# Kernel tuning notes

Measured on AMD Instinct MI355X. Metric: run time of the kernel, lower is better.

The kernel has to match this reference:

```python
import jax, jax.numpy as jnp
import numpy as np

N_NODES = 50000
N_EDGES = 1600000
D_IN = 512
D_OUT = 512


def setup_inputs() -> dict:
    key = jax.random.key(0)
    k1, k2, k3, k4, k5, k6 = jax.random.split(key, 6)
    stdv = 1.0 / np.sqrt(D_OUT)
    x = jax.random.normal(k1, (N_NODES, D_IN), dtype=jnp.float32)
    weight = jax.random.uniform(k2, (D_IN, D_OUT), dtype=jnp.float32, minval=-stdv, maxval=stdv)
    bias = jax.random.uniform(k3, (1, D_OUT), dtype=jnp.float32, minval=-stdv, maxval=stdv)
    edge_val = jax.random.uniform(k4, (N_EDGES,), dtype=jnp.float32)
    edge_row = jax.random.randint(k5, (N_EDGES,), 0, N_NODES, dtype=jnp.int64)
    edge_col = jax.random.randint(k6, (N_EDGES,), 0, N_NODES, dtype=jnp.int64)
    return {"x": x, "weight": weight, "bias": bias,
            "edge_val": edge_val, "edge_row": edge_row, "edge_col": edge_col}


def reference(x, weight, bias, edge_val, edge_row, edge_col):
    # hidden = X @ W  : [N, D_OUT] dense GEMM
    hidden = jnp.matmul(x, weight)
    # spmm: out[i] = sum over edges (i <- j) of adj_val * hidden[j]
    msgs = edge_val[:, None] * hidden[edge_col]            # [E, D_OUT]
    out = jax.ops.segment_sum(msgs, edge_row, num_segments=N_NODES)
    return out + bias
```

## Files before the change

kernel.cpp:

```cpp
#include <hip/hip_runtime.h>

typedef short short8 __attribute__((ext_vector_type(8)));
typedef float v4f   __attribute__((ext_vector_type(4)));

#define N_NODES 50000
#define N_EDGES 1600000
#define DIM     512
#define SCAN_NB 49

__device__ __forceinline__ float bf2f(unsigned short u) {
    unsigned int x = ((unsigned int)u) << 16;
    return __uint_as_float(x);
}
__device__ __forceinline__ unsigned short f2bf(float f) {
    unsigned int x = __float_as_uint(f);
    unsigned int r = x + 0x7fffu + ((x >> 16) & 1u);
    return (unsigned short)(r >> 16);
}

__global__ void detect_kernel(const unsigned int* __restrict__ xw,
                              const int* __restrict__ erow,
                              int* __restrict__ flags) {
    __shared__ int cbf, cz;
    if (threadIdx.x == 0) { cbf = 0; cz = 0; }
    __syncthreads();
    int lb = 0, lz = 0;
    for (int i = threadIdx.x; i < 1024; i += 256) {
        unsigned int w = xw[i];
        unsigned int e0 = (w >> 7) & 0xFFu;
        unsigned int e1 = (w >> 23) & 0xFFu;
        if (e0 >= 0x70u && e0 <= 0x8Fu && e1 >= 0x70u && e1 <= 0x8Fu) lb++;
        if (erow[2 * i + 1] == 0) lz++;
    }
    atomicAdd(&cbf, lb);
    atomicAdd(&cz, lz);
    __syncthreads();
    if (threadIdx.x == 0) {
        flags[0] = (cbf > 512) ? 1 : 0;
        flags[1] = (cz > 512) ? 1 : 0;
    }
}

__global__ void transpose_w(const void* __restrict__ Wv,
                            unsigned short* __restrict__ Wt,
                            const int* __restrict__ flags) {
    __shared__ unsigned short tile[32][33];
    const bool fb = flags[0] != 0;
    int bx = blockIdx.x * 32, by = blockIdx.y * 32;
    int tx = threadIdx.x, ty = threadIdx.y;
    if (fb) {
        const unsigned short* W = (const unsigned short*)Wv;
        for (int r = ty; r < 32; r += 8)
            tile[r][tx] = W[(by + r) * DIM + bx + tx];
    } else {
        const float* W = (const float*)Wv;
        for (int r = ty; r < 32; r += 8)
            tile[r][tx] = f2bf(W[(by + r) * DIM + bx + tx]);
    }
    __syncthreads();
    for (int r = ty; r < 32; r += 8)
        Wt[(bx + r) * DIM + by + tx] = tile[tx][r];
}

#define TM 128
#define TN 128
#define BK 32
#define LP 40

__global__ __launch_bounds__(256) void gemm_kernel(
        const void* __restrict__ Xv,
        const unsigned short* __restrict__ Wt,
        unsigned short* __restrict__ H,
        const int* __restrict__ flags) {
    __shared__ unsigned short lA[TM * LP];
    __shared__ unsigned short lB[TN * LP];

    const bool fb = flags[0] != 0;
    const unsigned short* Xb = (const unsigned short*)Xv;
    const float*          Xf = (const float*)Xv;

    const int t = threadIdx.x;
    const int mBase = blockIdx.y * TM;
    const int nBase = blockIdx.x * TN;
    const int w = t >> 6, lane = t & 63;
    const int lr = lane & 15, quad = lane >> 4;
    const int wr = w >> 1, wc = w & 1;

    v4f acc[4][4];
    #pragma unroll
    for (int i = 0; i < 4; ++i)
        #pragma unroll
        for (int j = 0; j < 4; ++j) acc[i][j] = (v4f)0.0f;

    for (int k0 = 0; k0 < DIM; k0 += BK) {
        #pragma unroll
        for (int rep = 0; rep < 2; ++rep) {
            int idx = rep * 256 + t;
            int r = idx >> 2;
            int cc = (idx & 3) * 8;
            int grow = mBase + r; if (grow >= N_NODES) grow = N_NODES - 1;
            size_t goff = (size_t)grow * DIM + k0 + cc;
            if (fb) {
                uint4 av = *(const uint4*)(Xb + goff);
                *(uint4*)(&lA[r * LP + cc]) = av;
            } else {
                float4 a0 = *(const float4*)(Xf + goff);
                float4 a1 = *(const float4*)(Xf + goff + 4);
                uint4 av;
                av.x = (unsigned int)f2bf(a0.x) | ((unsigned int)f2bf(a0.y) << 16);
                av.y = (unsigned int)f2bf(a0.z) | ((unsigned int)f2bf(a0.w) << 16);
                av.z = (unsigned int)f2bf(a1.x) | ((unsigned int)f2bf(a1.y) << 16);
                av.w = (unsigned int)f2bf(a1.z) | ((unsigned int)f2bf(a1.w) << 16);
                *(uint4*)(&lA[r * LP + cc]) = av;
            }
            uint4 bv = *(const uint4*)(Wt + (size_t)(nBase + r) * DIM + k0 + cc);
            *(uint4*)(&lB[r * LP + cc]) = bv;
        }
        __syncthreads();

        short8 bfr[4];
        #pragma unroll
        for (int j = 0; j < 4; ++j)
            bfr[j] = *(const short8*)(&lB[(wc * 64 + j * 16 + lr) * LP + quad * 8]);
        #pragma unroll
        for (int i = 0; i < 4; ++i) {
            short8 a = *(const short8*)(&lA[(wr * 64 + i * 16 + lr) * LP + quad * 8]);
            #pragma unroll
            for (int j = 0; j < 4; ++j)
                acc[i][j] = __builtin_amdgcn_mfma_f32_16x16x32_bf16(a, bfr[j], acc[i][j], 0, 0, 0);
        }
        __syncthreads();
    }

    #pragma unroll
    for (int i = 0; i < 4; ++i) {
        #pragma unroll
        for (int j = 0; j < 4; ++j) {
            #pragma unroll
            for (int r = 0; r < 4; ++r) {
                int gm = mBase + wr * 64 + i * 16 + quad * 4 + r;
                int gn = nBase + wc * 64 + j * 16 + lr;
                if (gm < N_NODES)
                    H[(size_t)gm * DIM + gn] = f2bf(acc[i][j][r]);
            }
        }
    }
}

__global__ void hist_kernel(const int* __restrict__ row, int* __restrict__ cnt,
                            const int* __restrict__ flags) {
    const bool f64 = flags[1] != 0;
    int i = blockIdx.x * 256 + threadIdx.x;
    if (i < N_EDGES) {
        int r = f64 ? row[2 * (size_t)i] : row[i];
        atomicAdd(&cnt[r], 1);
    }
}

__global__ __launch_bounds__(256) void scan1_kernel(const int* __restrict__ cnt,
                                                    int* __restrict__ bsum) {
    __shared__ int sh[256];
    const int b = blockIdx.x, t = threadIdx.x;
    int base = b * 1024 + t * 4;
    int s = 0;
    #pragma unroll
    for (int k = 0; k < 4; ++k) {
        int i = base + k;
        if (i < N_NODES) s += cnt[i];
    }
    sh[t] = s;
    __syncthreads();
    for (int off = 128; off > 0; off >>= 1) {
        if (t < off) sh[t] += sh[t + off];
        __syncthreads();
    }
    if (t == 0) bsum[b] = sh[0];
}

__global__ void scan2_kernel(const int* __restrict__ bsum, int* __restrict__ boff,
                             int* __restrict__ start) {
    if (threadIdx.x == 0) {
        int run = 0;
        for (int b = 0; b < SCAN_NB; ++b) { boff[b] = run; run += bsum[b]; }
        start[N_NODES] = N_EDGES;
    }
}

__global__ __launch_bounds__(256) void scan3_kernel(const int* __restrict__ cnt,
                                                    const int* __restrict__ boff,
                                                    int* __restrict__ start,
                                                    int* __restrict__ cursor) {
    __shared__ int sh[256];
    const int b = blockIdx.x, t = threadIdx.x;
    int base = b * 1024 + t * 4;
    int v[4];
    #pragma unroll
    for (int k = 0; k < 4; ++k) {
        int i = base + k;
        v[k] = (i < N_NODES) ? cnt[i] : 0;
    }
    int tsum = v[0] + v[1] + v[2] + v[3];
    sh[t] = tsum;
    __syncthreads();
    for (int off = 1; off < 256; off <<= 1) {
        int x = (t >= off) ? sh[t - off] : 0;
        __syncthreads();
        sh[t] += x;
        __syncthreads();
    }
    int excl = sh[t] - tsum + boff[b];
    #pragma unroll
    for (int k = 0; k < 4; ++k) {
        int i = base + k;
        if (i < N_NODES) { start[i] = excl; cursor[i] = excl; }
        excl += v[k];
    }
}

__global__ void scatter_kernel(const int* __restrict__ row, const int* __restrict__ col,
                               const void* __restrict__ valv,
                               int* __restrict__ cursor,
                               int2* __restrict__ sCV,
                               const int* __restrict__ flags) {
    const bool fb  = flags[0] != 0;
    const bool f64 = flags[1] != 0;
    int i = blockIdx.x * 256 + threadIdx.x;
    if (i < N_EDGES) {
        int r = f64 ? row[2 * (size_t)i] : row[i];
        int c = f64 ? col[2 * (size_t)i] : col[i];
        float v = fb ? bf2f(((const unsigned short*)valv)[i])
                     : ((const float*)valv)[i];
        int p = atomicAdd(&cursor[r], 1);
        int2 cv; cv.x = c; cv.y = __float_as_int(v);
        sCV[p] = cv;
    }
}

__global__ __launch_bounds__(256) void gather_kernel(
        const int* __restrict__ start, const int2* __restrict__ sCV,
        const unsigned short* __restrict__ H,
        const void* __restrict__ biasv, void* __restrict__ outv,
        const int* __restrict__ flags) {
    const bool fb = flags[0] != 0;
    const int node = blockIdx.x;
    const int t = threadIdx.x;
    const int s = start[node], e = start[node + 1];
    float a0 = 0.f, a1 = 0.f;
    #pragma unroll 4
    for (int p = s; p < e; ++p) {
        int2 cv = sCV[p];
        float v = __int_as_float(cv.y);
        unsigned int h = *(const unsigned int*)(H + (size_t)cv.x * DIM + t * 2);
        a0 = fmaf(v, bf2f((unsigned short)(h & 0xffffu)), a0);
        a1 = fmaf(v, bf2f((unsigned short)(h >> 16)), a1);
    }
    if (fb) {
        unsigned int bb = ((const unsigned int*)biasv)[t];
        a0 += bf2f((unsigned short)(bb & 0xffffu));
        a1 += bf2f((unsigned short)(bb >> 16));
        unsigned int o = (unsigned int)f2bf(a0) | ((unsigned int)f2bf(a1) << 16);
        ((unsigned int*)outv)[(size_t)node * (DIM / 2) + t] = o;
    } else {
        const float* bf = (const float*)biasv;
        a0 += bf[t * 2];
        a1 += bf[t * 2 + 1];
        float2 o; o.x = a0; o.y = a1;
        *(float2*)((float*)outv + (size_t)node * DIM + t * 2) = o;
    }
}

extern "C" void kernel_launch(void* const* d_in, const int* in_sizes, int n_in,
                              void* d_out, int out_size, void* d_ws, size_t ws_size,
                              hipStream_t stream) {
    const void* X    = d_in[0];
    const void* W    = d_in[1];
    const void* bias = d_in[2];
    const void* eval = d_in[3];
    const int*  erow = (const int*)d_in[4];
    const int*  ecol = (const int*)d_in[5];

    char* w = (char*)d_ws;
    size_t o = 0;
    int* flags = (int*)(w + o); o += 256;
    unsigned short* hidden = (unsigned short*)(w + o); o += (size_t)N_NODES * DIM * 2;
    int2*  sCV    = (int2*)(w + o);  o += (size_t)N_EDGES * 8;
    int*   cnt    = (int*)(w + o);   o += 200704;
    int*   start  = (int*)(w + o);   o += 200704;
    int*   cursor = (int*)(w + o);   o += 200704;
    unsigned short* Wt = (unsigned short*)(w + o); o += (size_t)DIM * DIM * 2;
    int*   bsum   = (int*)(w + o);   o += 256;
    int*   boff   = (int*)(w + o);   o += 256;

    hipMemsetAsync(cnt, 0, N_NODES * sizeof(int), stream);

    detect_kernel<<<1, 256, 0, stream>>>((const unsigned int*)X, erow, flags);
    transpose_w<<<dim3(16, 16), dim3(32, 8), 0, stream>>>(W, Wt, flags);
    gemm_kernel<<<dim3(DIM / TN, (N_NODES + TM - 1) / TM), 256, 0, stream>>>(X, Wt, hidden, flags);
    hist_kernel<<<(N_EDGES + 255) / 256, 256, 0, stream>>>(erow, cnt, flags);
    scan1_kernel<<<SCAN_NB, 256, 0, stream>>>(cnt, bsum);
    scan2_kernel<<<1, 64, 0, stream>>>(bsum, boff, start);
    scan3_kernel<<<SCAN_NB, 256, 0, stream>>>(cnt, boff, start, cursor);
    scatter_kernel<<<(N_EDGES + 255) / 256, 256, 0, stream>>>(erow, ecol, eval, cursor, sCV, flags);
    gather_kernel<<<N_NODES, 256, 0, stream>>>(start, sCV, hidden, bias, d_out, flags);
}
```

Baseline: 700.9 us.

## Pre-convert X to bf16, merge scan kernels, widen gather to 4 columns per thread

Adds a convert_x pass that writes X as bf16 into workspace once, so the GEMM reads bf16 instead of converting fp32 in each of its four column-block passes over X. The single-threaded scan2 kernel is folded into scan3, where each block sums the preceding block totals itself. The gather kernel now uses 128 threads per node, each loading and accumulating 4 bf16 values with vector loads and stores. Costs are an extra full read and write of X and a dependency on sufficient workspace size, which falls back to the old path if it is not available.

```diff
diff --git a/kernel.cpp b/kernel.cpp
--- a/kernel.cpp
+++ b/kernel.cpp
@@ -12,10 +12,10 @@
     unsigned int x = ((unsigned int)u) << 16;
     return __uint_as_float(x);
 }
-__device__ __forceinline__ unsigned short f2bf(float f) {
+__device__ __forceinline__ unsigned int f2bfu(float f) {
     unsigned int x = __float_as_uint(f);
     unsigned int r = x + 0x7fffu + ((x >> 16) & 1u);
-    return (unsigned short)(r >> 16);
+    return r >> 16;
 }
 
 __global__ void detect_kernel(const unsigned int* __restrict__ xw,
@@ -39,6 +39,22 @@
         flags[0] = (cbf > 512) ? 1 : 0;
         flags[1] = (cz > 512) ? 1 : 0;
     }
+}
+
+__global__ __launch_bounds__(256) void convert_x(const void* __restrict__ Xv,
+                                                 unsigned short* __restrict__ Xc,
+                                                 const int* __restrict__ flags) {
+    if (flags[0] != 0) return;
+    const float* Xf = (const float*)Xv;
+    size_t i = ((size_t)blockIdx.x * 256 + threadIdx.x) * 8;
+    float4 f0 = *(const float4*)(Xf + i);
+    float4 f1 = *(const float4*)(Xf + i + 4);
+    uint4 o;
+    o.x = f2bfu(f0.x) | (f2bfu(f0.y) << 16);
+    o.y = f2bfu(f0.z) | (f2bfu(f0.w) << 16);
+    o.z = f2bfu(f1.x) | (f2bfu(f1.y) << 16);
+    o.w = f2bfu(f1.z) | (f2bfu(f1.w) << 16);
+    *(uint4*)(Xc + i) = o;
 }
 
 __global__ void transpose_w(const void* __restrict__ Wv,
@@ -55,7 +71,7 @@
     } else {
         const float* W = (const float*)Wv;
         for (int r = ty; r < 32; r += 8)
-            tile[r][tx] = f2bf(W[(by + r) * DIM + bx + tx]);
+            tile[r][tx] = (unsigned short)f2bfu(W[(by + r) * DIM + bx + tx]);
     }
     __syncthreads();
     for (int r = ty; r < 32; r += 8)
@@ -69,6 +85,8 @@
 
 __global__ __launch_bounds__(256) void gemm_kernel(
         const void* __restrict__ Xv,
+        const unsigned short* __restrict__ Xc,
+        const int have_xc,
         const unsigned short* __restrict__ Wt,
         unsigned short* __restrict__ H,
         const int* __restrict__ flags) {
@@ -76,7 +94,8 @@
     __shared__ unsigned short lB[TN * LP];
 
     const bool fb = flags[0] != 0;
-    const unsigned short* Xb = (const unsigned short*)Xv;
+    const bool bfp = fb || (have_xc != 0);
+    const unsigned short* Xb = fb ? (const unsigned short*)Xv : Xc;
     const float*          Xf = (const float*)Xv;
 
     const int t = threadIdx.x;
@@ -100,17 +119,17 @@
             int cc = (idx & 3) * 8;
             int grow = mBase + r; if (grow >= N_NODES) grow = N_NODES - 1;
             size_t goff = (size_t)grow * DIM + k0 + cc;
-            if (fb) {
+            if (bfp) {
                 uint4 av = *(const uint4*)(Xb + goff);
                 *(uint4*)(&lA[r * LP + cc]) = av;
             } else {
                 float4 a0 = *(const float4*)(Xf + goff);
                 float4 a1 = *(const float4*)(Xf + goff + 4);
                 uint4 av;
-                av.x = (unsigned int)f2bf(a0.x) | ((unsigned int)f2bf(a0.y) << 16);
-                av.y = (unsigned int)f2bf(a0.z) | ((unsigned int)f2bf(a0.w) << 16);
-                av.z = (unsigned int)f2bf(a1.x) | ((unsigned int)f2bf(a1.y) << 16);
-                av.w = (unsigned int)f2bf(a1.z) | ((unsigned int)f2bf(a1.w) << 16);
+                av.x = f2bfu(a0.x) | (f2bfu(a0.y) << 16);
+                av.y = f2bfu(a0.z) | (f2bfu(a0.w) << 16);
+                av.z = f2bfu(a1.x) | (f2bfu(a1.y) << 16);
+                av.w = f2bfu(a1.z) | (f2bfu(a1.w) << 16);
                 *(uint4*)(&lA[r * LP + cc]) = av;
             }
             uint4 bv = *(const uint4*)(Wt + (size_t)(nBase + r) * DIM + k0 + cc);
@@ -141,7 +160,7 @@
                 int gm = mBase + wr * 64 + i * 16 + quad * 4 + r;
                 int gn = nBase + wc * 64 + j * 16 + lr;
                 if (gm < N_NODES)
-                    H[(size_t)gm * DIM + gn] = f2bf(acc[i][j][r]);
+                    H[(size_t)gm * DIM + gn] = (unsigned short)f2bfu(acc[i][j][r]);
             }
         }
     }
@@ -177,21 +196,20 @@
     if (t == 0) bsum[b] = sh[0];
 }
 
-__global__ void scan2_kernel(const int* __restrict__ bsum, int* __restrict__ boff,
-                             int* __restrict__ start) {
-    if (threadIdx.x == 0) {
-        int run = 0;
-        for (int b = 0; b < SCAN_NB; ++b) { boff[b] = run; run += bsum[b]; }
-        start[N_NODES] = N_EDGES;
-    }
-}
-
 __global__ __launch_bounds__(256) void scan3_kernel(const int* __restrict__ cnt,
-                                                    const int* __restrict__ boff,
+                                                    const int* __restrict__ bsum,
                                                     int* __restrict__ start,
                                                     int* __restrict__ cursor) {
     __shared__ int sh[256];
+    __shared__ int boffs;
     const int b = blockIdx.x, t = threadIdx.x;
+    if (t == 0) {
+        int r = 0;
+        #pragma unroll 8
+        for (int i = 0; i < b; ++i) r += bsum[i];
+        boffs = r;
+        if (b == 0) start[N_NODES] = N_EDGES;
+    }
     int base = b * 1024 + t * 4;
     int v[4];
     #pragma unroll
@@ -208,7 +226,7 @@
         sh[t] += x;
         __syncthreads();
     }
-    int excl = sh[t] - tsum + boff[b];
+    int excl = sh[t] - tsum + boffs;
     #pragma unroll
     for (int k = 0; k < 4; ++k) {
         int i = base + k;
@@ -236,7 +254,7 @@
     }
 }
 
-__global__ __launch_bounds__(256) void gather_kernel(
+__global__ __launch_bounds__(128) void gather_kernel(
         const int* __restrict__ start, const int2* __restrict__ sCV,
         const unsigned short* __restrict__ H,
         const void* __restrict__ biasv, void* __restrict__ outv,
@@ -245,27 +263,32 @@
     const int node = blockIdx.x;
     const int t = threadIdx.x;
     const int s = start[node], e = start[node + 1];
-    float a0 = 0.f, a1 = 0.f;
+    float a0 = 0.f, a1 = 0.f, a2 = 0.f, a3 = 0.f;
     #pragma unroll 4
     for (int p = s; p < e; ++p) {
         int2 cv = sCV[p];
         float v = __int_as_float(cv.y);
-        unsigned int h = *(const unsigned int*)(H + (size_t)cv.x * DIM + t * 2);
-        a0 = fmaf(v, bf2f((unsigned short)(h & 0xffffu)), a0);
-        a1 = fmaf(v, bf2f((unsigned short)(h >> 16)), a1);
+        uint2 h = *(const uint2*)(H + (size_t)cv.x * DIM + t * 4);
+        a0 = fmaf(v, bf2f((unsigned short)(h.x & 0xffffu)), a0);
+        a1 = fmaf(v, bf2f((unsigned short)(h.x >> 16)), a1);
+        a2 = fmaf(v, bf2f((unsigned short)(h.y & 0xffffu)), a2);
+        a3 = fmaf(v, bf2f((unsigned short)(h.y >> 16)), a3);
     }
     if (fb) {
-        unsigned int bb = ((const unsigned int*)biasv)[t];
-        a0 += bf2f((unsigned short)(bb & 0xffffu));
-        a1 += bf2f((unsigned short)(bb >> 16));
-        unsigned int o = (unsigned int)f2bf(a0) | ((unsigned int)f2bf(a1) << 16);
-        ((unsigned int*)outv)[(size_t)node * (DIM / 2) + t] = o;
+        uint2 bb = ((const uint2*)biasv)[t];
+        a0 += bf2f((unsigned short)(bb.x & 0xffffu));
+        a1 += bf2f((unsigned short)(bb.x >> 16));
+        a2 += bf2f((unsigned short)(bb.y & 0xffffu));
+        a3 += bf2f((unsigned short)(bb.y >> 16));
+        uint2 o;
+        o.x = f2bfu(a0) | (f2bfu(a1) << 16);
+        o.y = f2bfu(a2) | (f2bfu(a3) << 16);
+        *(uint2*)((unsigned short*)outv + (size_t)node * DIM + t * 4) = o;
     } else {
-        const float* bf = (const float*)biasv;
-        a0 += bf[t * 2];
-        a1 += bf[t * 2 + 1];
-        float2 o; o.x = a0; o.y = a1;
-        *(float2*)((float*)outv + (size_t)node * DIM + t * 2) = o;
+        float4 bb = ((const float4*)biasv)[t];
+        float4 o;
+        o.x = a0 + bb.x; o.y = a1 + bb.y; o.z = a2 + bb.z; o.w = a3 + bb.w;
+        *(float4*)((float*)outv + (size_t)node * DIM + t * 4) = o;
     }
 }
 
@@ -289,17 +312,22 @@
     int*   cursor = (int*)(w + o);   o += 200704;
     unsigned short* Wt = (unsigned short*)(w + o); o += (size_t)DIM * DIM * 2;
     int*   bsum   = (int*)(w + o);   o += 256;
-    int*   boff   = (int*)(w + o);   o += 256;
+    size_t base_end = o;
+    unsigned short* Xc = (unsigned short*)(w + o);
+    size_t need_xc = base_end + (size_t)N_NODES * DIM * 2;
+    const int have_xc = (ws_size >= need_xc) ? 1 : 0;
 
     hipMemsetAsync(cnt, 0, N_NODES * sizeof(int), stream);
 
     detect_kernel<<<1, 256, 0, stream>>>((const unsigned int*)X, erow, flags);
+    if (have_xc)
+        convert_x<<<(N_NODES * DIM) / (256 * 8), 256, 0, stream>>>(X, Xc, flags);
     transpose_w<<<dim3(16, 16), dim3(32, 8), 0, stream>>>(W, Wt, flags);
-    gemm_kernel<<<dim3(DIM / TN, (N_NODES + TM - 1) / TM), 256, 0, stream>>>(X, Wt, hidden, flags);
+    gemm_kernel<<<dim3(DIM / TN, (N_NODES + TM - 1) / TM), 256, 0, stream>>>(
+        X, Xc, have_xc, Wt, hidden, flags);
     hist_kernel<<<(N_EDGES + 255) / 256, 256, 0, stream>>>(erow, cnt, flags);
     scan1_kernel<<<SCAN_NB, 256, 0, stream>>>(cnt, bsum);
-    scan2_kernel<<<1, 64, 0, stream>>>(bsum, boff, start);
-    scan3_kernel<<<SCAN_NB, 256, 0, stream>>>(cnt, boff, start, cursor);
+    scan3_kernel<<<SCAN_NB, 256, 0, stream>>>(cnt, bsum, start, cursor);
     scatter_kernel<<<(N_EDGES + 255) / 256, 256, 0, stream>>>(erow, ecol, eval, cursor, sCV, flags);
-    gather_kernel<<<N_NODES, 256, 0, stream>>>(start, sCV, hidden, bias, d_out, flags);
-}
+    gather_kernel<<<N_NODES, 128, 0, stream>>>(start, sCV, hidden, bias, d_out, flags);
+}
```

Measured after the change: 690.7 us. Within noise of the previous version (-1.5%).
